# Optimization experiments

Measured on AMD Instinct MI355X. Metric: run time of the kernel, lower is better.

## Reference

```python
import jax, jax.numpy as jnp
import numpy as np

B, T, C = 2, 2048, 2048
H, KV, D = 16, 4, 128   # n_head, n_kv_head, head_dim
EPS = 1.1920929e-07     # torch.finfo(float32).eps, F.rms_norm default


def setup_inputs() -> dict:
    key = jax.random.key(0)
    ks = jax.random.split(key, 7)
    x = jax.random.normal(ks[0], (B, T, C), dtype=jnp.float32)
    # rope angles: cos/sin of positions, broadcastable to [B,T,H,D//2]
    inv_freq = 1.0 / (10000.0 ** (jnp.arange(0, D // 2, dtype=jnp.float32) / (D // 2)))
    ang = jnp.arange(T, dtype=jnp.float32)[:, None] * inv_freq[None, :]
    cos = jnp.cos(ang)[None, :, None, :]  # [1,T,1,D/2]
    sin = jnp.sin(ang)[None, :, None, :]
    s = 0.02
    Wq = jax.random.normal(ks[1], (C, H * D), dtype=jnp.float32) * s
    Wk = jax.random.normal(ks[2], (C, KV * D), dtype=jnp.float32) * s
    Wv = jax.random.normal(ks[3], (C, KV * D), dtype=jnp.float32) * s
    Wo = jax.random.normal(ks[4], (C, C), dtype=jnp.float32) * s
    return {"x": x, "cos": cos, "sin": sin, "Wq": Wq, "Wk": Wk, "Wv": Wv, "Wo": Wo}


def _rope(t, cos, sin):
    d = t.shape[-1] // 2
    t1, t2 = t[..., :d], t[..., d:]
    return jnp.concatenate([t1 * cos + t2 * sin, -t1 * sin + t2 * cos], axis=-1)


def _rmsnorm(t):
    return t * jax.lax.rsqrt(jnp.mean(t * t, axis=-1, keepdims=True) + EPS)


def reference(x, cos, sin, Wq, Wk, Wv, Wo):
    q = (x @ Wq).reshape(B, T, H, D)
    k = (x @ Wk).reshape(B, T, KV, D)
    v = (x @ Wv).reshape(B, T, KV, D)
    q = _rmsnorm(_rope(q, cos, sin))
    k = _rmsnorm(_rope(k, cos, sin))
    # [B, KV, G, T, D] query grouped per kv head (GQA)
    G = H // KV
    qh = q.transpose(0, 2, 1, 3).reshape(B, KV, G, T, D)
    kh = k.transpose(0, 2, 1, 3)  # [B, KV, T, D]
    vh = v.transpose(0, 2, 1, 3)
    scale = 1.0 / np.sqrt(D).astype(np.float32)
    scores = jnp.einsum('bhgqd,bhkd->bhgqk', qh, kh) * scale
    causal = jnp.tril(jnp.ones((T, T), dtype=bool))
    scores = jnp.where(causal, scores, jnp.finfo(scores.dtype).min)
    attn = jax.nn.softmax(scores, axis=-1)
    y = jnp.einsum('bhgqk,bhkd->bhgqd', attn, vh)  # [B,KV,G,T,D]
    y = y.reshape(B, H, T, D).transpose(0, 2, 1, 3).reshape(B, T, C)
    return y @ Wo
```

## Files before the change

### kernel.cpp

```cpp
#include <hip/hip_runtime.h>

using bf16x8 = __attribute__((ext_vector_type(8))) short;
using f32x4  = __attribute__((ext_vector_type(4))) float;

#define B_  2
#define T_  2048
#define C_  2048
#define H_  16
#define KV_ 4
#define D_  128

__device__ __forceinline__ unsigned short f2b(float f) {
  union { float f; unsigned int u; } v; v.f = f;
  unsigned int r = v.u + 0x7fffu + ((v.u >> 16) & 1u);
  return (unsigned short)(r >> 16);
}
__device__ __forceinline__ float b2f(unsigned short u) {
  union { unsigned int u; float f; } v; v.u = ((unsigned int)u) << 16;
  return v.f;
}
__device__ __forceinline__ unsigned int cvt_pk_bf16(float lo, float hi) {
  unsigned int r;
  asm("v_cvt_pk_bf16_f32 %0, %1, %2" : "=v"(r) : "v"(lo), "v"(hi));
  return r;
}
__device__ __forceinline__ void gld_lds16(const void* g, void* l) {
  __builtin_amdgcn_global_load_lds(
      (__attribute__((address_space(1))) void*)g,
      (__attribute__((address_space(3))) void*)l, 16, 0, 0);
}

__global__ void prep(const float* __restrict__ x, unsigned short* __restrict__ xb,
                     const float* __restrict__ Wq, const float* __restrict__ Wk,
                     const float* __restrict__ Wv, const float* __restrict__ Wo,
                     unsigned short* __restrict__ Wqt, unsigned short* __restrict__ Wkt,
                     unsigned short* __restrict__ Wvt, unsigned short* __restrict__ Wot) {
  __shared__ float s[32][33];
  int bid = blockIdx.x, tid = threadIdx.x;
  if (bid < 8192) {
    int i = bid * 256 + tid;
    float4 f = ((const float4*)x)[i];
    ushort4 u; u.x = f2b(f.x); u.y = f2b(f.y); u.z = f2b(f.z); u.w = f2b(f.w);
    ((ushort4*)xb)[i] = u;
    return;
  }
  int id = bid - 8192;
  const float* W; unsigned short* Wt; int N;
  if (id < 4096)      { W = Wq; Wt = Wqt; N = 2048; }
  else if (id < 5120) { W = Wk; Wt = Wkt; N = 512;  id -= 4096; }
  else if (id < 6144) { W = Wv; Wt = Wvt; N = 512;  id -= 5120; }
  else                { W = Wo; Wt = Wot; N = 2048; id -= 6144; }
  int ntiles = N >> 5;
  int n0 = (id % ntiles) * 32, k0 = (id / ntiles) * 32;
  int tx = tid & 31, ty = tid >> 5;
  #pragma unroll
  for (int yy = 0; yy < 32; yy += 8)
    s[ty + yy][tx] = W[(size_t)(k0 + ty + yy) * N + n0 + tx];
  __syncthreads();
  #pragma unroll
  for (int yy = 0; yy < 32; yy += 8)
    Wt[(size_t)(n0 + ty + yy) * 2048 + k0 + tx] = f2b(s[tx][ty + yy]);
}

__global__ __launch_bounds__(512, 2) void qkv_gemm2p(
    const unsigned short* __restrict__ xb,
    const unsigned short* __restrict__ Wt,
    unsigned short* __restrict__ qkv) {
  __shared__ unsigned short lds[57344];

  const int id  = (int)blockIdx.x;
  const int xcd = id & 7, j = id >> 3;
  const int mt  = xcd * 2 + (j >> 4);
  const int nt  = j & 15;
  const int m0 = mt * 256, n0 = nt * 192;

  const int tid = (int)threadIdx.x;
  const int w = tid >> 6, lane = tid & 63;
  const int quad = lane >> 4, l16 = lane & 15;
  const int wr = w >> 1, wc = w & 1;
  const int swz = (l16 & 12) << 1;

  const unsigned short* Ab = xb + (size_t)m0 * 2048;
  const unsigned short* Bb = Wt + (size_t)n0 * 2048;

  int ar[4], axc[4];
  #pragma unroll
  for (int kq = 0; kq < 4; ++kq) {
    int ca = tid + kq * 512;
    ar[kq]  = (ca & 1023) >> 2;
    axc[kq] = ((ca & 3) * 8) ^ ((((ca & 1023) >> 4) & 3) << 3);
  }
  const int khb1 = (tid < 256) ? 0 : 1;
  int bidx[3] = { tid, tid + 512 - khb1 * 768, tid + 256 };
  int bkh[3]  = { 0, khb1, 1 };
  int br[3], bxc[3];
  #pragma unroll
  for (int kq = 0; kq < 3; ++kq) {
    br[kq]  = bidx[kq] >> 2;
    bxc[kq] = ((bidx[kq] & 3) * 8) ^ (((bidx[kq] >> 4) & 3) << 3);
  }

#define STAGE(buf, kb) do { \
    unsigned short* da_ = lds + (buf) * 16384; \
    _Pragma("unroll") \
    for (int kq = 0; kq < 4; ++kq) { \
      int ca_ = tid + kq * 512; \
      gld_lds16(Ab + (size_t)ar[kq] * 2048 + (kb) + (ca_ >> 10) * 32 + axc[kq], da_ + ca_ * 8); \
    } \
    unsigned short* db_ = lds + 32768 + (buf) * 12288; \
    _Pragma("unroll") \
    for (int kq = 0; kq < 3; ++kq) \
      gld_lds16(Bb + (size_t)br[kq] * 2048 + (kb) + bkh[kq] * 32 + bxc[kq], \
                db_ + bkh[kq] * 6144 + bidx[kq] * 8); \
  } while (0)

  f32x4 acc[4][6] = {};

  STAGE(0, 0);
  __syncthreads();

  const unsigned short* aB = lds + (wr * 64 + l16) * 32 + (quad * 8 ^ swz);
  const unsigned short* bB = lds + 32768 + (wc * 96 + l16) * 32 + (quad * 8 ^ swz);

  for (int t = 0; t < 32; ++t) {
    const int cur = t & 1;
    if (t < 31) STAGE(cur ^ 1, (t + 1) * 64);
    #pragma unroll
    for (int kh = 0; kh < 2; ++kh) {
      bf16x8 a[4], b[6];
      #pragma unroll
      for (int m = 0; m < 4; ++m)
        a[m] = *(const bf16x8*)(aB + cur * 16384 + kh * 8192 + m * 512);
      #pragma unroll
      for (int n = 0; n < 6; ++n)
        b[n] = *(const bf16x8*)(bB + cur * 12288 + kh * 6144 + n * 512);
      #pragma unroll
      for (int m = 0; m < 4; ++m)
        #pragma unroll
        for (int n = 0; n < 6; ++n)
          acc[m][n] = __builtin_amdgcn_mfma_f32_16x16x32_bf16(a[m], b[n], acc[m][n], 0, 0, 0);
    }
    __syncthreads();
  }
#undef STAGE

  #pragma unroll
  for (int m = 0; m < 4; ++m)
    #pragma unroll
    for (int r = 0; r < 4; ++r) {
      int row = m0 + wr * 64 + m * 16 + quad * 4 + r;
      #pragma unroll
      for (int n = 0; n < 6; ++n) {
        int col = n0 + wc * 96 + n * 16 + l16;
        qkv[(size_t)row * 3072 + col] = f2b(acc[m][n][r]);
      }
    }
}

__global__ __launch_bounds__(512, 2) void out_gemm2p(
    const unsigned short* __restrict__ yb,
    const unsigned short* __restrict__ Wot,
    float* __restrict__ out) {
  __shared__ unsigned short lds[49152];

  const int id  = (int)blockIdx.x;
  const int xcd = id & 7, j = id >> 3;
  const int mt  = xcd * 2 + (j >> 4);
  const int nt  = j & 15;
  const int m0 = mt * 256, n0 = nt * 128;

  const int tid = (int)threadIdx.x;
  const int w = tid >> 6, lane = tid & 63;
  const int quad = lane >> 4, l16 = lane & 15;
  const int wr = w >> 1, wc = w & 1;
  const int swz = (l16 & 12) << 1;

  const unsigned short* Ab = yb  + (size_t)m0 * 2048;
  const unsigned short* Bb = Wot + (size_t)n0 * 2048;

  int ar[4], axc[4];
  #pragma unroll
  for (int kq = 0; kq < 4; ++kq) {
    int ca = tid + kq * 512;
    ar[kq]  = (ca & 1023) >> 2;
    axc[kq] = ((ca & 3) * 8) ^ ((((ca & 1023) >> 4) & 3) << 3);
  }
  int brr[2], bxc[2];
  #pragma unroll
  for (int kq = 0; kq < 2; ++kq) {
    int cb = tid + kq * 512;
    brr[kq] = (cb & 511) >> 2;
    bxc[kq] = ((cb & 3) * 8) ^ ((((cb & 511) >> 4) & 3) << 3);
  }

#define STAGE(buf, kb) do { \
    unsigned short* da_ = lds + (buf) * 16384; \
    _Pragma("unroll") \
    for (int kq = 0; kq < 4; ++kq) { \
      int ca_ = tid + kq * 512; \
      gld_lds16(Ab + (size_t)ar[kq] * 2048 + (kb) + (ca_ >> 10) * 32 + axc[kq], da_ + ca_ * 8); \
    } \
    unsigned short* db_ = lds + 32768 + (buf) * 8192; \
    _Pragma("unroll") \
    for (int kq = 0; kq < 2; ++kq) { \
      int cb_ = tid + kq * 512; \
      gld_lds16(Bb + (size_t)brr[kq] * 2048 + (kb) + kq * 32 + bxc[kq], db_ + cb_ * 8); \
    } \
  } while (0)

  f32x4 acc[4][4] = {};

  STAGE(0, 0);
  __syncthreads();

  const unsigned short* aB = lds + (wr * 64 + l16) * 32 + (quad * 8 ^ swz);
  const unsigned short* bB = lds + 32768 + (wc * 64 + l16) * 32 + (quad * 8 ^ swz);

  for (int t = 0; t < 32; ++t) {
    const int cur = t & 1;
    if (t < 31) STAGE(cur ^ 1, (t + 1) * 64);
    #pragma unroll
    for (int kh = 0; kh < 2; ++kh) {
      bf16x8 a[4], b[4];
      #pragma unroll
      for (int m = 0; m < 4; ++m)
        a[m] = *(const bf16x8*)(aB + cur * 16384 + kh * 8192 + m * 512);
      #pragma unroll
      for (int n = 0; n < 4; ++n)
        b[n] = *(const bf16x8*)(bB + cur * 8192 + kh * 4096 + n * 512);
      #pragma unroll
      for (int m = 0; m < 4; ++m)
        #pragma unroll
        for (int n = 0; n < 4; ++n)
          acc[m][n] = __builtin_amdgcn_mfma_f32_16x16x32_bf16(a[m], b[n], acc[m][n], 0, 0, 0);
    }
    __syncthreads();
  }
#undef STAGE

  #pragma unroll
  for (int m = 0; m < 4; ++m)
    #pragma unroll
    for (int r = 0; r < 4; ++r) {
      int row = m0 + wr * 64 + m * 16 + quad * 4 + r;
      #pragma unroll
      for (int n = 0; n < 4; ++n) {
        int col = n0 + wc * 64 + n * 16 + l16;
        out[(size_t)row * 2048 + col] = acc[m][n][r];
      }
    }
}

template <int NH>
__device__ __forceinline__ void ropenorm_row(
    const unsigned short* __restrict__ in, const float* __restrict__ cs,
    const float* __restrict__ sn, unsigned short* __restrict__ out,
    float oscale, int off, int row, int lane) {
  int head = row % NH;
  int t = (row / NH) & (T_ - 1);
  int b = row / (NH * T_);
  const unsigned short* p = in + (size_t)(b * T_ + t) * 3072 + off + head * D_;
  unsigned int u  = *(const unsigned int*)(p + 2 * lane);
  unsigned int up = (unsigned int)__shfl_xor((int)u, 32, 64);
  int dh = (lane & 31) * 2;
  float2 c2 = ((const float2*)(cs + t * 64))[lane & 31];
  float2 s2 = ((const float2*)(sn + t * 64))[lane & 31];
  float a0 = b2f((unsigned short)(u & 0xffff)),  a1 = b2f((unsigned short)(u >> 16));
  float p0 = b2f((unsigned short)(up & 0xffff)), p1 = b2f((unsigned short)(up >> 16));
  float sgn = (lane < 32) ? 1.0f : -1.0f;
  float oa = a0 * c2.x + sgn * p0 * s2.x;
  float ob = a1 * c2.y + sgn * p1 * s2.y;
  float ss = oa * oa + ob * ob;
  #pragma unroll
  for (int off2 = 32; off2 > 0; off2 >>= 1) ss += __shfl_xor(ss, off2, 64);
  float r = rsqrtf(ss * (1.0f / 128.0f) + 1.1920929e-07f) * oscale;
  unsigned int outu = cvt_pk_bf16(oa * r, ob * r);
  size_t base = ((size_t)((b * NH + head) * 128 + (t >> 4))) * 2048 + (size_t)(t & 15) * 8;
  int f = ((lane < 32) ? 0 : 8) + (dh >> 3);
  *(unsigned int*)(out + base + (size_t)f * 128 + (dh & 7)) = outu;
}

__global__ void post_k(const unsigned short* __restrict__ qkv,
                       const float* __restrict__ cs, const float* __restrict__ sn,
                       unsigned short* __restrict__ qfr, unsigned short* __restrict__ kfr,
                       unsigned short* __restrict__ vf) {
  int bid = blockIdx.x, tid = threadIdx.x;
  int lane = tid & 63, wv = tid >> 6;
  if (bid < 16384) {
    ropenorm_row<16>(qkv, cs, sn, qfr, 0.08838834764831845f, 0, bid * 4 + wv, lane);
    return;
  }
  if (bid < 20480) {
    ropenorm_row<4>(qkv, cs, sn, kfr, 1.0f, 2048, (bid - 16384) * 4 + wv, lane);
    return;
  }
  int id = bid - 20480;
  int it = id & 31, y = id >> 5;
  int b = y >> 2, kv = y & 3;
  int d = tid & 127, ty = tid >> 7;
  int t0 = it * 64;
  size_t obase = ((size_t)((b * KV_ + kv) * 32 + it)) * 8192
               + (size_t)(d >> 4) * 1024 + (size_t)(d & 15) * 8;
  #pragma unroll
  for (int tcg = 0; tcg < 4; ++tcg) {
    int tc = ty * 4 + tcg;
    unsigned short val[8];
    #pragma unroll
    for (int e = 0; e < 8; ++e)
      val[e] = qkv[((size_t)(b * T_) + t0 + tc * 8 + e) * 3072 + 2560 + kv * D_ + d];
    ushort4 u0 = {val[0], val[1], val[2], val[3]};
    ushort4 u1 = {val[4], val[5], val[6], val[7]};
    *(ushort4*)(vf + obase + (size_t)tc * 128)     = u0;
    *(ushort4*)(vf + obase + (size_t)tc * 128 + 4) = u1;
  }
}

__global__ __launch_bounds__(512, 2) void attn_kernel(
    const unsigned short* __restrict__ qf, const unsigned short* __restrict__ kf,
    const unsigned short* __restrict__ vf, unsigned short* __restrict__ yb) {
  __shared__ __align__(16) char smem[135168];
  unsigned short* kls = (unsigned short*)smem;
  unsigned short* vls = (unsigned short*)(smem + 65536);
  unsigned short* Pls = (unsigned short*)(smem + 98304);

  const int xp = (int)blockIdx.x, b = xp >> 2, kv = xp & 3;
  const int jy = (int)blockIdx.y;
  const int tid = (int)threadIdx.x;
  const int w = tid >> 6, lane = tid & 63;
  const int quad = lane >> 4, l16 = lane & 15;
  const int hh = w & 3, half = w >> 2;
  const int h = kv * 4 + hh;
  unsigned short* myP = Pls + w * (32 * 72);

  const unsigned short* Kf = kf + (size_t)(b * KV_ + kv) * 128 * 2048;
  const unsigned short* Vf = vf + (size_t)(b * KV_ + kv) * 32 * 8192;

  const int swl = quad << 4;
  const int cs0 = (tid * 8) ^ swl;
  const int cs1 = ((tid + 512) * 8) ^ swl;
  const int cd0 = tid * 8, cd1 = tid * 8 + 4096;

#define STAGE_K(buf, it0) do { \
    const unsigned short* s_ = Kf + (size_t)(it0) * 8192; \
    unsigned short* d_ = kls + (buf) * 16384; \
    gld_lds16(s_ + cs0, d_ + cd0);               gld_lds16(s_ + cs1, d_ + cd1); \
    gld_lds16(s_ + 8192 + cs0, d_ + 8192 + cd0); gld_lds16(s_ + 8192 + cs1, d_ + 8192 + cd1); \
  } while (0)
#define STAGE_V(it0) do { \
    const unsigned short* s_ = Vf + (size_t)(it0) * 8192; \
    gld_lds16(s_ + cs0, vls + cd0);               gld_lds16(s_ + cs1, vls + cd1); \
    gld_lds16(s_ + 8192 + cs0, vls + 8192 + cd0); gld_lds16(s_ + 8192 + cs1, vls + 8192 + cd1); \
  } while (0)

  for (int ph = 0; ph < 2; ++ph) {
    const int qt = ph ? (63 - jy) : jy;
    const int q0 = qt * 32;
    const int ntile = (qt >> 1) + 1;
    const int R = (ntile + 1) >> 1;

    const unsigned short* Qf = qf + ((size_t)(b * H_ + h) * 128 + qt * 2) * 2048;
    bf16x8 bq[2][4];
    #pragma unroll
    for (int i = 0; i < 2; ++i)
      #pragma unroll
      for (int kk = 0; kk < 4; ++kk)
        bq[i][kk] = *(const bf16x8*)(Qf + (size_t)i * 2048 + (kk * 4 + quad) * 128 + l16 * 8);

    float l_i[2] = {0.f, 0.f};
    f32x4 o[2][8] = {};

    STAGE_K(0, 0);

    for (int r = 0; r < R; ++r) {
      const int cur = r & 1;
      const bool more = (r + 1 < R);
      STAGE_V(2 * r);
      if (more) STAGE_K(cur ^ 1, 2 * r + 2);
      if (more) asm volatile("s_waitcnt vmcnt(8)" ::: "memory");
      else      asm volatile("s_waitcnt vmcnt(4)" ::: "memory");
      __builtin_amdgcn_s_barrier();

      const int it = 2 * r + half;
      const bool active = it < ntile;
      f32x4 sc[4][2] = {};
      if (active) {
        const unsigned short* kb = kls + cur * 16384 + half * 8192;
        #pragma unroll
        for (int kk = 0; kk < 4; ++kk) {
          bf16x8 ak[4];
          #pragma unroll
          for (int jt = 0; jt < 4; ++jt)
            ak[jt] = *(const bf16x8*)(kb + ((jt * 2048 + (kk * 4 + quad) * 128 + l16 * 8) ^ swl));
          #pragma unroll
          for (int jt = 0; jt < 4; ++jt)
            #pragma unroll
            for (int i = 0; i < 2; ++i)
              sc[jt][i] = __builtin_amdgcn_mfma_f32_16x16x32_bf16(ak[jt], bq[i][kk], sc[jt][i], 0, 0, 0);
        }
        if (it == ntile - 1) {
          #pragma unroll
          for (int jt = 0; jt < 4; ++jt) {
            int kg = it * 64 + jt * 16 + quad * 4;
            #pragma unroll
            for (int i = 0; i < 2; ++i) {
              int qg = q0 + i * 16 + l16;
              #pragma unroll
              for (int rr = 0; rr < 4; ++rr)
                if (kg + rr > qg) sc[jt][i][rr] = -3.0e38f;
            }
          }
        }
        #pragma unroll
        for (int i = 0; i < 2; ++i) {
          float part = 0.f;
          #pragma unroll
          for (int jt = 0; jt < 4; ++jt)
            #pragma unroll
            for (int rr = 0; rr < 4; ++rr) {
              float p = __expf(sc[jt][i][rr] - 12.0f);
              sc[jt][i][rr] = p; part += p;
            }
          l_i[i] += part;
        }
        #pragma unroll
        for (int i = 0; i < 2; ++i)
          #pragma unroll
          for (int jt = 0; jt < 4; ++jt) {
            uint2 uu;
            uu.x = cvt_pk_bf16(sc[jt][i][0], sc[jt][i][1]);
            uu.y = cvt_pk_bf16(sc[jt][i][2], sc[jt][i][3]);
            *(uint2*)(myP + (i * 16 + l16) * 72 + jt * 16 + quad * 4) = uu;
          }
      }

      if (more) asm volatile("s_waitcnt vmcnt(4)" ::: "memory");
      else      asm volatile("s_waitcnt vmcnt(0)" ::: "memory");
      __builtin_amdgcn_s_barrier();

      if (active) {
        const unsigned short* vb = vls + half * 8192;
        #pragma unroll
        for (int kk2 = 0; kk2 < 2; ++kk2) {
          bf16x8 ap[2], bv2[8];
          #pragma unroll
          for (int i = 0; i < 2; ++i)
            ap[i] = *(const bf16x8*)(myP + (i * 16 + l16) * 72 + kk2 * 32 + quad * 8);
          #pragma unroll
          for (int jj = 0; jj < 8; ++jj)
            bv2[jj] = *(const bf16x8*)(vb + ((jj * 1024 + (kk2 * 4 + quad) * 128 + l16 * 8) ^ swl));
          #pragma unroll
          for (int i = 0; i < 2; ++i)
            #pragma unroll
            for (int jj = 0; jj < 8; ++jj)
              o[i][jj] = __builtin_amdgcn_mfma_f32_16x16x32_bf16(ap[i], bv2[jj], o[i][jj], 0, 0, 0);
        }
      }
      __builtin_amdgcn_s_barrier();
    }

    float lsum[2];
    #pragma unroll
    for (int i = 0; i < 2; ++i) {
      float l = l_i[i];
      l += __shfl_xor(l, 16, 64);
      l += __shfl_xor(l, 32, 64);
      lsum[i] = l;
    }

    __syncthreads();
    float* oc = (float*)smem + hh * 4256;
    float* lc = oc + 32 * 132;
    if (half == 1) {
      #pragma unroll
      for (int i = 0; i < 2; ++i) {
        if (quad == 0) lc[i * 16 + l16] = lsum[i];
        #pragma unroll
        for (int jj = 0; jj < 8; ++jj)
          #pragma unroll
          for (int rr = 0; rr < 4; ++rr)
            oc[(i * 16 + quad * 4 + rr) * 132 + jj * 16 + l16] = o[i][jj][rr];
      }
    }
    __syncthreads();
    if (half == 0) {
      #pragma unroll
      for (int i = 0; i < 2; ++i) {
        float l = lsum[i] + lc[i * 16 + l16];
        float linv = 1.0f / l;
        float lr[4];
        #pragma unroll
        for (int rr = 0; rr < 4; ++rr) lr[rr] = __shfl(linv, quad * 4 + rr, 64);
        #pragma unroll
        for (int rr = 0; rr < 4; ++rr) {
          int tg = q0 + i * 16 + quad * 4 + rr;
          unsigned short* yr = yb + (((size_t)(b * T_ + tg)) * H_ + h) * D_;
          #pragma unroll
          for (int jj = 0; jj < 8; ++jj) {
            float vsum = o[i][jj][rr] + oc[(i * 16 + quad * 4 + rr) * 132 + jj * 16 + l16];
            yr[jj * 16 + l16] = f2b(vsum * lr[rr]);
          }
        }
      }
    }
    __syncthreads();
  }
#undef STAGE_K
#undef STAGE_V
}

extern "C" void kernel_launch(void* const* d_in, const int* in_sizes, int n_in,
                              void* d_out, int out_size, void* d_ws, size_t ws_size,
                              hipStream_t stream) {
  (void)in_sizes; (void)n_in; (void)out_size; (void)ws_size;
  const float* x  = (const float*)d_in[0];
  const float* cs = (const float*)d_in[1];
  const float* sn = (const float*)d_in[2];
  const float* Wq = (const float*)d_in[3];
  const float* Wk = (const float*)d_in[4];
  const float* Wv = (const float*)d_in[5];
  const float* Wo = (const float*)d_in[6];
  float* out = (float*)d_out;
  char* ws = (char*)d_ws;

  unsigned short* xb     = (unsigned short*)(ws + 0);
  unsigned short* Wqkvt  = (unsigned short*)(ws + 16777216);
  unsigned short* Wot    = (unsigned short*)(ws + 29360128);
  unsigned short* qkvcat = (unsigned short*)(ws + 37748736);
  unsigned short* qfr    = (unsigned short*)(ws + 62914560);
  unsigned short* kfr    = (unsigned short*)(ws + 79691776);
  unsigned short* vfr    = (unsigned short*)(ws + 83886080);
  unsigned short* yb     = xb;

  prep<<<dim3(18432), dim3(256), 0, stream>>>(
      x, xb, Wq, Wk, Wv, Wo,
      Wqkvt, Wqkvt + (size_t)2048 * 2048, Wqkvt + (size_t)2560 * 2048, Wot);
  qkv_gemm2p<<<dim3(256), dim3(512), 0, stream>>>(xb, Wqkvt, qkvcat);
  post_k<<<dim3(20736), dim3(256), 0, stream>>>(qkvcat, cs, sn, qfr, kfr, vfr);
  attn_kernel<<<dim3(8, 32), dim3(512), 0, stream>>>(qfr, kfr, vfr, yb);
  out_gemm2p<<<dim3(256), dim3(512), 0, stream>>>(yb, Wot, out);
}
```

Before: 280.9 us.

## Split attention work across query sub-tiles instead of key-tile halves

The attention kernel moves from 512-thread blocks, where two wave groups each handled half of the key tiles and merged their partial outputs through shared memory, to 256-thread blocks that each own a 16-row query sub-tile and walk every key tile sequentially. This drops the cross-half reduction, shrinks LDS per block, and doubles the grid to 512 blocks for better occupancy and load balance. The trade-off is that each K/V tile is loaded by twice as many blocks and each MFMA now has only one query sub-tile to reuse its K/V fragments, which lowers arithmetic intensity.

```diff
diff --git a/kernel.cpp b/kernel.cpp
--- a/kernel.cpp
+++ b/kernel.cpp
@@ -315,194 +315,139 @@
   }
 }
 
-__global__ __launch_bounds__(512, 2) void attn_kernel(
+__global__ __launch_bounds__(256, 2) void attn_kernel(
     const unsigned short* __restrict__ qf, const unsigned short* __restrict__ kf,
     const unsigned short* __restrict__ vf, unsigned short* __restrict__ yb) {
-  __shared__ __align__(16) char smem[135168];
+  __shared__ __align__(16) char smem[58368];
   unsigned short* kls = (unsigned short*)smem;
-  unsigned short* vls = (unsigned short*)(smem + 65536);
-  unsigned short* Pls = (unsigned short*)(smem + 98304);
+  unsigned short* vls = (unsigned short*)(smem + 32768);
+  unsigned short* Pls = (unsigned short*)(smem + 49152);
 
   const int xp = (int)blockIdx.x, b = xp >> 2, kv = xp & 3;
-  const int jy = (int)blockIdx.y;
+  const int yp = (int)blockIdx.y;
+  const int j = yp >> 1, sub = yp & 1;
   const int tid = (int)threadIdx.x;
   const int w = tid >> 6, lane = tid & 63;
   const int quad = lane >> 4, l16 = lane & 15;
-  const int hh = w & 3, half = w >> 2;
-  const int h = kv * 4 + hh;
-  unsigned short* myP = Pls + w * (32 * 72);
+  const int h = kv * 4 + w;
+  unsigned short* myP = Pls + w * (16 * 72);
 
   const unsigned short* Kf = kf + (size_t)(b * KV_ + kv) * 128 * 2048;
   const unsigned short* Vf = vf + (size_t)(b * KV_ + kv) * 32 * 8192;
 
   const int swl = quad << 4;
-  const int cs0 = (tid * 8) ^ swl;
-  const int cs1 = ((tid + 512) * 8) ^ swl;
-  const int cd0 = tid * 8, cd1 = tid * 8 + 4096;
 
 #define STAGE_K(buf, it0) do { \
     const unsigned short* s_ = Kf + (size_t)(it0) * 8192; \
-    unsigned short* d_ = kls + (buf) * 16384; \
-    gld_lds16(s_ + cs0, d_ + cd0);               gld_lds16(s_ + cs1, d_ + cd1); \
-    gld_lds16(s_ + 8192 + cs0, d_ + 8192 + cd0); gld_lds16(s_ + 8192 + cs1, d_ + 8192 + cd1); \
+    unsigned short* d_ = kls + (buf) * 8192; \
+    _Pragma("unroll") \
+    for (int q_ = 0; q_ < 4; ++q_) \
+      gld_lds16(s_ + ((tid * 8 + q_ * 2048) ^ swl), d_ + tid * 8 + q_ * 2048); \
   } while (0)
 #define STAGE_V(it0) do { \
     const unsigned short* s_ = Vf + (size_t)(it0) * 8192; \
-    gld_lds16(s_ + cs0, vls + cd0);               gld_lds16(s_ + cs1, vls + cd1); \
-    gld_lds16(s_ + 8192 + cs0, vls + 8192 + cd0); gld_lds16(s_ + 8192 + cs1, vls + 8192 + cd1); \
+    _Pragma("unroll") \
+    for (int q_ = 0; q_ < 4; ++q_) \
+      gld_lds16(s_ + ((tid * 8 + q_ * 2048) ^ swl), vls + tid * 8 + q_ * 2048); \
   } while (0)
 
   for (int ph = 0; ph < 2; ++ph) {
-    const int qt = ph ? (63 - jy) : jy;
-    const int q0 = qt * 32;
+    const int qt = ph ? (63 - j) : j;
+    const int q0 = qt * 32 + sub * 16;
     const int ntile = (qt >> 1) + 1;
-    const int R = (ntile + 1) >> 1;
-
-    const unsigned short* Qf = qf + ((size_t)(b * H_ + h) * 128 + qt * 2) * 2048;
-    bf16x8 bq[2][4];
-    #pragma unroll
-    for (int i = 0; i < 2; ++i)
-      #pragma unroll
-      for (int kk = 0; kk < 4; ++kk)
-        bq[i][kk] = *(const bf16x8*)(Qf + (size_t)i * 2048 + (kk * 4 + quad) * 128 + l16 * 8);
-
-    float l_i[2] = {0.f, 0.f};
-    f32x4 o[2][8] = {};
+
+    const unsigned short* Qf = qf + ((size_t)(b * H_ + h) * 128 + qt * 2 + sub) * 2048;
+    bf16x8 bq[4];
+    #pragma unroll
+    for (int kk = 0; kk < 4; ++kk)
+      bq[kk] = *(const bf16x8*)(Qf + (kk * 4 + quad) * 128 + l16 * 8);
+
+    float l_i = 0.f;
+    f32x4 o[8] = {};
 
     STAGE_K(0, 0);
 
-    for (int r = 0; r < R; ++r) {
+    for (int r = 0; r < ntile; ++r) {
       const int cur = r & 1;
-      const bool more = (r + 1 < R);
-      STAGE_V(2 * r);
-      if (more) STAGE_K(cur ^ 1, 2 * r + 2);
+      const bool more = (r + 1 < ntile);
+      STAGE_V(r);
+      if (more) STAGE_K(cur ^ 1, r + 1);
       if (more) asm volatile("s_waitcnt vmcnt(8)" ::: "memory");
       else      asm volatile("s_waitcnt vmcnt(4)" ::: "memory");
       __builtin_amdgcn_s_barrier();
 
-      const int it = 2 * r + half;
-      const bool active = it < ntile;
-      f32x4 sc[4][2] = {};
-      if (active) {
-        const unsigned short* kb = kls + cur * 16384 + half * 8192;
-        #pragma unroll
-        for (int kk = 0; kk < 4; ++kk) {
-          bf16x8 ak[4];
+      f32x4 sc[4] = {};
+      const unsigned short* kb = kls + cur * 8192;
+      #pragma unroll
+      for (int kk = 0; kk < 4; ++kk) {
+        bf16x8 ak[4];
+        #pragma unroll
+        for (int jt = 0; jt < 4; ++jt)
+          ak[jt] = *(const bf16x8*)(kb + ((jt * 2048 + (kk * 4 + quad) * 128 + l16 * 8) ^ swl));
+        #pragma unroll
+        for (int jt = 0; jt < 4; ++jt)
+          sc[jt] = __builtin_amdgcn_mfma_f32_16x16x32_bf16(ak[jt], bq[kk], sc[jt], 0, 0, 0);
+      }
+      if (r == ntile - 1) {
+        #pragma unroll
+        for (int jt = 0; jt < 4; ++jt) {
+          int kg = r * 64 + jt * 16 + quad * 4;
+          int qg = q0 + l16;
           #pragma unroll
-          for (int jt = 0; jt < 4; ++jt)
-            ak[jt] = *(const bf16x8*)(kb + ((jt * 2048 + (kk * 4 + quad) * 128 + l16 * 8) ^ swl));
-          #pragma unroll
-          for (int jt = 0; jt < 4; ++jt)
-            #pragma unroll
-            for (int i = 0; i < 2; ++i)
-              sc[jt][i] = __builtin_amdgcn_mfma_f32_16x16x32_bf16(ak[jt], bq[i][kk], sc[jt][i], 0, 0, 0);
+          for (int rr = 0; rr < 4; ++rr)
+            if (kg + rr > qg) sc[jt][rr] = -3.0e38f;
         }
-        if (it == ntile - 1) {
-          #pragma unroll
-          for (int jt = 0; jt < 4; ++jt) {
-            int kg = it * 64 + jt * 16 + quad * 4;
-            #pragma unroll
-            for (int i = 0; i < 2; ++i) {
-              int qg = q0 + i * 16 + l16;
-              #pragma unroll
-              for (int rr = 0; rr < 4; ++rr)
-                if (kg + rr > qg) sc[jt][i][rr] = -3.0e38f;
-            }
-          }
+      }
+      float part = 0.f;
+      #pragma unroll
+      for (int jt = 0; jt < 4; ++jt)
+        #pragma unroll
+        for (int rr = 0; rr < 4; ++rr) {
+          float p = __expf(sc[jt][rr] - 12.0f);
+          sc[jt][rr] = p; part += p;
         }
-        #pragma unroll
-        for (int i = 0; i < 2; ++i) {
-          float part = 0.f;
-          #pragma unroll
-          for (int jt = 0; jt < 4; ++jt)
-            #pragma unroll
-            for (int rr = 0; rr < 4; ++rr) {
-              float p = __expf(sc[jt][i][rr] - 12.0f);
-              sc[jt][i][rr] = p; part += p;
-            }
-          l_i[i] += part;
-        }
-        #pragma unroll
-        for (int i = 0; i < 2; ++i)
-          #pragma unroll
-          for (int jt = 0; jt < 4; ++jt) {
-            uint2 uu;
-            uu.x = cvt_pk_bf16(sc[jt][i][0], sc[jt][i][1]);
-            uu.y = cvt_pk_bf16(sc[jt][i][2], sc[jt][i][3]);
-            *(uint2*)(myP + (i * 16 + l16) * 72 + jt * 16 + quad * 4) = uu;
-          }
+      l_i += part;
+      #pragma unroll
+      for (int jt = 0; jt < 4; ++jt) {
+        uint2 uu;
+        uu.x = cvt_pk_bf16(sc[jt][0], sc[jt][1]);
+        uu.y = cvt_pk_bf16(sc[jt][2], sc[jt][3]);
+        *(uint2*)(myP + l16 * 72 + jt * 16 + quad * 4) = uu;
       }
 
       if (more) asm volatile("s_waitcnt vmcnt(4)" ::: "memory");
       else      asm volatile("s_waitcnt vmcnt(0)" ::: "memory");
       __builtin_amdgcn_s_barrier();
 
-      if (active) {
-        const unsigned short* vb = vls + half * 8192;
-        #pragma unroll
-        for (int kk2 = 0; kk2 < 2; ++kk2) {
-          bf16x8 ap[2], bv2[8];
-          #pragma unroll
-          for (int i = 0; i < 2; ++i)
-            ap[i] = *(const bf16x8*)(myP + (i * 16 + l16) * 72 + kk2 * 32 + quad * 8);
-          #pragma unroll
-          for (int jj = 0; jj < 8; ++jj)
-            bv2[jj] = *(const bf16x8*)(vb + ((jj * 1024 + (kk2 * 4 + quad) * 128 + l16 * 8) ^ swl));
-          #pragma unroll
-          for (int i = 0; i < 2; ++i)
-            #pragma unroll
-            for (int jj = 0; jj < 8; ++jj)
-              o[i][jj] = __builtin_amdgcn_mfma_f32_16x16x32_bf16(ap[i], bv2[jj], o[i][jj], 0, 0, 0);
-        }
+      #pragma unroll
+      for (int kk2 = 0; kk2 < 2; ++kk2) {
+        bf16x8 ap = *(const bf16x8*)(myP + l16 * 72 + kk2 * 32 + quad * 8);
+        bf16x8 bv2[8];
+        #pragma unroll
+        for (int jj = 0; jj < 8; ++jj)
+          bv2[jj] = *(const bf16x8*)(vls + ((jj * 1024 + (kk2 * 4 + quad) * 128 + l16 * 8) ^ swl));
+        #pragma unroll
+        for (int jj = 0; jj < 8; ++jj)
+          o[jj] = __builtin_amdgcn_mfma_f32_16x16x32_bf16(ap, bv2[jj], o[jj], 0, 0, 0);
       }
       __builtin_amdgcn_s_barrier();
     }
 
-    float lsum[2];
-    #pragma unroll
-    for (int i = 0; i < 2; ++i) {
-      float l = l_i[i];
-      l += __shfl_xor(l, 16, 64);
-      l += __shfl_xor(l, 32, 64);
-      lsum[i] = l;
-    }
-
-    __syncthreads();
-    float* oc = (float*)smem + hh * 4256;
-    float* lc = oc + 32 * 132;
-    if (half == 1) {
-      #pragma unroll
-      for (int i = 0; i < 2; ++i) {
-        if (quad == 0) lc[i * 16 + l16] = lsum[i];
-        #pragma unroll
-        for (int jj = 0; jj < 8; ++jj)
-          #pragma unroll
-          for (int rr = 0; rr < 4; ++rr)
-            oc[(i * 16 + quad * 4 + rr) * 132 + jj * 16 + l16] = o[i][jj][rr];
-      }
-    }
-    __syncthreads();
-    if (half == 0) {
-      #pragma unroll
-      for (int i = 0; i < 2; ++i) {
-        float l = lsum[i] + lc[i * 16 + l16];
-        float linv = 1.0f / l;
-        float lr[4];
-        #pragma unroll
-        for (int rr = 0; rr < 4; ++rr) lr[rr] = __shfl(linv, quad * 4 + rr, 64);
-        #pragma unroll
-        for (int rr = 0; rr < 4; ++rr) {
-          int tg = q0 + i * 16 + quad * 4 + rr;
-          unsigned short* yr = yb + (((size_t)(b * T_ + tg)) * H_ + h) * D_;
-          #pragma unroll
-          for (int jj = 0; jj < 8; ++jj) {
-            float vsum = o[i][jj][rr] + oc[(i * 16 + quad * 4 + rr) * 132 + jj * 16 + l16];
-            yr[jj * 16 + l16] = f2b(vsum * lr[rr]);
-          }
-        }
-      }
-    }
-    __syncthreads();
+    float l = l_i;
+    l += __shfl_xor(l, 16, 64);
+    l += __shfl_xor(l, 32, 64);
+    float linv = 1.0f / l;
+    float lr[4];
+    #pragma unroll
+    for (int rr = 0; rr < 4; ++rr) lr[rr] = __shfl(linv, quad * 4 + rr, 64);
+    #pragma unroll
+    for (int rr = 0; rr < 4; ++rr) {
+      int tg = q0 + quad * 4 + rr;
+      unsigned short* yr = yb + (((size_t)(b * T_ + tg)) * H_ + h) * D_;
+      #pragma unroll
+      for (int jj = 0; jj < 8; ++jj)
+        yr[jj * 16 + l16] = f2b(o[jj][rr] * lr[rr]);
+    }
   }
 #undef STAGE_K
 #undef STAGE_V
@@ -536,6 +481,6 @@
       Wqkvt, Wqkvt + (size_t)2048 * 2048, Wqkvt + (size_t)2560 * 2048, Wot);
   qkv_gemm2p<<<dim3(256), dim3(512), 0, stream>>>(xb, Wqkvt, qkvcat);
   post_k<<<dim3(20736), dim3(256), 0, stream>>>(qkvcat, cs, sn, qfr, kfr, vfr);
-  attn_kernel<<<dim3(8, 32), dim3(512), 0, stream>>>(qfr, kfr, vfr, yb);
+  attn_kernel<<<dim3(8, 64), dim3(256), 0, stream>>>(qfr, kfr, vfr, yb);
   out_gemm2p<<<dim3(256), dim3(512), 0, stream>>>(yb, Wot, out);
 }
```

Result: no change. 278.3 us (median of 3 runs) (-0.9%).
